# Performance work log

Measured on AMD Instinct MI355X. Metric: run time of the kernel, lower is better.

## Reference

```python
import jax, jax.numpy as jnp
import numpy as np
from jax import lax

B, T, O, E, I = 256, 16, 32, 32, 32
H, HL = 64, 64  # edge_dim, latent_edge_dim
TE, EI = T * E, E + I


def _mlp(x, layers):
    for w, b in layers[:-1]:
        x = jax.nn.relu(x @ w + b)
    w, b = layers[-1]
    return x @ w + b


def _get_edges(x, layers):
    # x: [B, O, D]; antisymmetric pairwise aggregation over upper-triangular pairs
    Bn, On, D = x.shape
    ii, jj = np.triu_indices(On, 1)  # static indices, P = O(O-1)/2
    pair_in = jnp.concatenate([x[:, ii, :], x[:, jj, :]], axis=-1)  # [B, P, 2D]
    e = _mlp(pair_in, layers)  # [B, P, H_out]
    agg = jnp.zeros((Bn, On, e.shape[-1]), x.dtype)
    agg = agg.at[:, ii, :].add(e).at[:, jj, :].add(-e)
    return agg


def setup_inputs() -> dict:
    key = jax.random.key(0)
    ks = iter(jax.random.split(key, 64))

    def lin(din, dout):
        w = jax.random.normal(next(ks), (din, dout), jnp.float32) * (1.0 / np.sqrt(din)).astype(np.float32)
        b = jnp.zeros((dout,), jnp.float32)
        return w, b

    inp = {"z_explicit_seq": jax.random.normal(next(ks), (B, T, O, E), jnp.float32)}
    groups = {
        "ee": [(2 * TE, 64), (64, 64), (64, H)],
        "ne": [(TE + H, 64), (64, 64), (64, 32), (32, I)],
        "le": [(2 * EI, 64), (64, 64), (64, HL)],
        "lt": [(EI + HL, 64), (64, 64), (64, 32), (32, 16), (16, EI)],
    }
    for name, dims in groups.items():
        for k, (din, dout) in enumerate(dims, start=1):
            w, b = lin(din, dout)
            inp[f"{name}{k}_w"] = w
            inp[f"{name}{k}_b"] = b
    inp["t_future"] = 8
    return inp


def reference(z_explicit_seq,
              ee1_w, ee1_b, ee2_w, ee2_b, ee3_w, ee3_b,
              ne1_w, ne1_b, ne2_w, ne2_b, ne3_w, ne3_b, ne4_w, ne4_b,
              le1_w, le1_b, le2_w, le2_b, le3_w, le3_b,
              lt1_w, lt1_b, lt2_w, lt2_b, lt3_w, lt3_b, lt4_w, lt4_b, lt5_w, lt5_b,
              t_future):
    ee = [(ee1_w, ee1_b), (ee2_w, ee2_b), (ee3_w, ee3_b)]
    ne = [(ne1_w, ne1_b), (ne2_w, ne2_b), (ne3_w, ne3_b), (ne4_w, ne4_b)]
    le = [(le1_w, le1_b), (le2_w, le2_b), (le3_w, le3_b)]
    lt = [(lt1_w, lt1_b), (lt2_w, lt2_b), (lt3_w, lt3_b), (lt4_w, lt4_b), (lt5_w, lt5_b)]

    z = z_explicit_seq  # [B, T, O, E]
    # define_source: first frame + temporal diffs, flatten time into features
    src = jnp.concatenate([z[:, :1], z[:, 1:] - z[:, :-1]], axis=1)  # [B,T,O,E]
    src = jnp.transpose(src, (0, 2, 1, 3)).reshape(B, O, TE)  # [B,O,TE]

    edge_agg = _get_edges(src, ee)  # [B,O,H]
    z_impl = _mlp(jnp.concatenate([src, edge_agg], axis=-1), ne)  # [B,O,I]
    z_cur = jnp.concatenate([z[:, -1], z_impl], axis=-1)  # [B,O,EI]

    def step(zc, _):
        agg = _get_edges(zc, le)  # [B,O,HL]
        delta = _mlp(jnp.concatenate([zc, agg], axis=-1), lt)  # [B,O,EI]
        zn = zc + delta
        return zn, zn[..., :E]

    _, preds = lax.scan(step, z_cur, None, length=t_future)  # [t,B,O,E]
    return jnp.transpose(preds, (1, 0, 2, 3))  # [B,t_future,O,E]
```

## Files before the change

### kernel.cpp

```cpp
#include <hip/hip_runtime.h>

#define NB 256
#define NO 32
#define NEE 32
#define NT 16
#define THREADS 512

typedef const float* __restrict__ fp;

struct Params {
  fp z;
  fp ee1w, ee1b, ee2w, ee2b, ee3w, ee3b;
  fp ne1w, ne1b, ne2w, ne2b, ne3w, ne3b, ne4w, ne4b;
  fp le1w, le1b, le2w, le2b, le3w, le3b;
  fp lt1w, lt1b, lt2w, lt2b, lt3w, lt3b, lt4w, lt4b, lt5w, lt5b;
  float* out;
  int tf;
};

__device__ __forceinline__ float frelu(float x) { return x > 0.f ? x : 0.f; }

__device__ __forceinline__ float rl(float v, int l) {
  return __uint_as_float(__builtin_amdgcn_readlane(__float_as_uint(v), l));
}

#define OFF_UT  0
#define OFF_VT  2112
#define OFF_AG  4224
#define OFF_BN  6272
#define OFF_NW  8320
#define LDSF    16000

__device__ __forceinline__ void stageN(float* dst, const float* __restrict__ src,
                                       int nf4, int tid) {
  for (int i4 = tid; i4 < nf4; i4 += THREADS)
    *(float4*)(dst + i4 * 4) = *(const float4*)(src + i4 * 4);
}

template<int KC>
__device__ __forceinline__ void dense4L(const float* x0, const float* x1,
                                        const float* x2, const float* x3,
                                        const float* __restrict__ w, int ldw,
                                        int col, float o[4]) {
#pragma unroll 4
  for (int kc = 0; kc < KC; ++kc) {
    float w0 = w[(4 * kc + 0) * ldw + col];
    float w1 = w[(4 * kc + 1) * ldw + col];
    float w2 = w[(4 * kc + 2) * ldw + col];
    float w3 = w[(4 * kc + 3) * ldw + col];
    float4 a = *(const float4*)(x0 + 4 * kc);
    float4 b = *(const float4*)(x1 + 4 * kc);
    float4 c = *(const float4*)(x2 + 4 * kc);
    float4 d = *(const float4*)(x3 + 4 * kc);
    o[0] = fmaf(a.x, w0, o[0]); o[0] = fmaf(a.y, w1, o[0]); o[0] = fmaf(a.z, w2, o[0]); o[0] = fmaf(a.w, w3, o[0]);
    o[1] = fmaf(b.x, w0, o[1]); o[1] = fmaf(b.y, w1, o[1]); o[1] = fmaf(b.z, w2, o[1]); o[1] = fmaf(b.w, w3, o[1]);
    o[2] = fmaf(c.x, w0, o[2]); o[2] = fmaf(c.y, w1, o[2]); o[2] = fmaf(c.z, w2, o[2]); o[2] = fmaf(c.w, w3, o[2]);
    o[3] = fmaf(d.x, w0, o[3]); o[3] = fmaf(d.y, w1, o[3]); o[3] = fmaf(d.z, w2, o[3]); o[3] = fmaf(d.w, w3, o[3]);
  }
}

__global__ __attribute__((amdgpu_waves_per_eu(2, 2)))
__launch_bounds__(THREADS) void rld_kernel(Params P) {
  __shared__ float lds[LDSF];
  const int b = blockIdx.x;
  const int tid = (int)threadIdx.x;
  const int lane = tid & 63;
  const int wave = tid >> 6;
  const int cc = lane & 31;
  const int c16 = lane & 15;

  float* UT = lds + OFF_UT;
  float* VT = lds + OFF_VT;
  float* AG = lds + OFF_AG;
  float* sBn = lds + OFF_BN + wave * 256;
  float* src = lds + OFF_BN;
  const float* wlt2 = lds + OFF_NW;
  const float* wlt3 = lds + OFF_NW + 4096;
  const float* wlt4 = lds + OFF_NW + 6144;
  const float* wlt5 = lds + OFF_NW + 6656;
  const int i0 = wave, i1 = wave + 8, i2 = wave + 16, i3 = wave + 24;
  const int h33 = lane * 33;
  const float* zb = P.z + (size_t)b * NT * NO * NEE;

  stageN(lds + OFF_NW,        P.lt2w, 1024, tid);
  stageN(lds + OFF_NW + 4096, P.lt3w,  512, tid);
  stageN(lds + OFF_NW + 6144, P.lt4w,  128, tid);
  stageN(lds + OFF_NW + 6656, P.lt5w,  256, tid);

  float au[4] = {0,0,0,0}, av[4] = {0,0,0,0}, s1r[4] = {0,0,0,0};
  for (int qq = 0; qq < 8; ++qq) {
    __syncthreads();
    for (int idx = tid; idx < 2048; idx += THREADS) {
      int i = idx >> 6, kk = idx & 63;
      int k = qq * 64 + kk, t = k >> 5, e = k & 31;
      float v = zb[(t * NO + i) * NEE + e];
      if (t > 0) v -= zb[((t - 1) * NO + i) * NEE + e];
      src[i * 64 + kk] = v;
    }
    __syncthreads();
    for (int c = 0; c < 2; ++c) {
      int r0 = qq * 64 + c * 32;
      const float* x0 = src + i0 * 64 + c * 32;
      const float* x1 = src + i1 * 64 + c * 32;
      const float* x2 = src + i2 * 64 + c * 32;
      const float* x3 = src + i3 * 64 + c * 32;
      dense4L<8>(x0, x1, x2, x3, P.ee1w + (size_t)r0 * 64,         64, lane, au);
      dense4L<8>(x0, x1, x2, x3, P.ee1w + (size_t)(512 + r0) * 64, 64, lane, av);
      dense4L<8>(x0, x1, x2, x3, P.ne1w + (size_t)r0 * 64,         64, lane, s1r);
    }
  }
  {
    float eb1 = P.ee1b[lane];
    UT[h33 + i0] = au[0] + eb1; UT[h33 + i1] = au[1] + eb1;
    UT[h33 + i2] = au[2] + eb1; UT[h33 + i3] = au[3] + eb1;
    VT[h33 + i0] = av[0]; VT[h33 + i1] = av[1];
    VT[h33 + i2] = av[2]; VT[h33 + i3] = av[3];
  }
  for (int z = tid; z < 2048; z += THREADS) AG[z] = 0.f;

  float w2c[64], w3c[64];
#pragma unroll
  for (int h = 0; h < 64; ++h) w2c[h] = P.ee2w[h * 64 + lane];
#pragma unroll
  for (int h = 0; h < 64; ++h) w3c[h] = P.ee3w[h * 64 + lane];
  float b2c = P.ee2b[lane], b3c = P.ee3b[lane];
  __syncthreads();

  const int tf = P.tf;
  float zci[4] = {0, 0, 0, 0};
  float* outb = P.out + (size_t)b * tf * NO * NEE;

  for (int s = 0; s <= tf; ++s) {
    {
      int pi = 0, rem = wave * 62;
      while (rem >= 31 - pi) { rem -= 31 - pi; ++pi; }
      int pj = pi + 1 + rem;
#pragma unroll 1
      for (int pp = 0; pp < 31; ++pp) {
        const int iA = pi, jA = pj;
        ++pj; if (pj == 32) { ++pi; pj = pi + 1; }
        const int iB = pi, jB = pj;
        ++pj; if (pj == 32) { ++pi; pj = pi + 1; }
        float xA = fmaxf(UT[h33 + iA] + VT[h33 + jA], 0.f);
        float xB = fmaxf(UT[h33 + iB] + VT[h33 + jB], 0.f);
        float a0 = b2c, a1 = 0.f, c0 = b2c, c1 = 0.f;
#pragma unroll
        for (int h = 0; h < 64; h += 2) {
          a0 = fmaf(rl(xA, h),     w2c[h],     a0);
          a1 = fmaf(rl(xA, h + 1), w2c[h + 1], a1);
          c0 = fmaf(rl(xB, h),     w2c[h],     c0);
          c1 = fmaf(rl(xB, h + 1), w2c[h + 1], c1);
        }
        float yA = fmaxf(a0 + a1, 0.f);
        float yB = fmaxf(c0 + c1, 0.f);
        float e0 = b3c, e1 = 0.f, f0 = b3c, f1 = 0.f;
#pragma unroll
        for (int h = 0; h < 64; h += 2) {
          e0 = fmaf(rl(yA, h),     w3c[h],     e0);
          e1 = fmaf(rl(yA, h + 1), w3c[h + 1], e1);
          f0 = fmaf(rl(yB, h),     w3c[h],     f0);
          f1 = fmaf(rl(yB, h + 1), w3c[h + 1], f1);
        }
        float eA = e0 + e1, eB = f0 + f1;
        atomicAdd(&AG[iA * 64 + lane],  eA);
        atomicAdd(&AG[jA * 64 + lane], -eA);
        atomicAdd(&AG[iB * 64 + lane],  eB);
        atomicAdd(&AG[jB * 64 + lane], -eB);
      }
    }
    __syncthreads();

    if (s == 0) {
      float nb1 = P.ne1b[lane], nb2 = P.ne2b[lane];
      float nb3 = P.ne3b[cc],   nb4 = P.ne4b[cc];
      float o1[4] = {s1r[0] + nb1, s1r[1] + nb1, s1r[2] + nb1, s1r[3] + nb1};
      dense4L<16>(AG + i0 * 64, AG + i1 * 64, AG + i2 * 64, AG + i3 * 64,
                  P.ne1w + (size_t)512 * 64, 64, lane, o1);
      sBn[lane] = frelu(o1[0]); sBn[64 + lane] = frelu(o1[1]);
      sBn[128 + lane] = frelu(o1[2]); sBn[192 + lane] = frelu(o1[3]);
      float o2[4] = {nb2, nb2, nb2, nb2};
      dense4L<16>(sBn, sBn + 64, sBn + 128, sBn + 192, P.ne2w, 64, lane, o2);
      sBn[lane] = frelu(o2[0]); sBn[64 + lane] = frelu(o2[1]);
      sBn[128 + lane] = frelu(o2[2]); sBn[192 + lane] = frelu(o2[3]);
      float o3[4] = {nb3, nb3, nb3, nb3};
      dense4L<16>(sBn, sBn + 64, sBn + 128, sBn + 192, P.ne3w, 32, cc, o3);
      sBn[cc] = frelu(o3[0]); sBn[64 + cc] = frelu(o3[1]);
      sBn[128 + cc] = frelu(o3[2]); sBn[192 + cc] = frelu(o3[3]);
      float o4[4] = {nb4, nb4, nb4, nb4};
      dense4L<8>(sBn, sBn + 64, sBn + 128, sBn + 192, P.ne4w, 32, cc, o4);
      zci[0] = (lane < 32) ? zb[(15 * NO + i0) * NEE + lane] : o4[0];
      zci[1] = (lane < 32) ? zb[(15 * NO + i1) * NEE + lane] : o4[1];
      zci[2] = (lane < 32) ? zb[(15 * NO + i2) * NEE + lane] : o4[2];
      zci[3] = (lane < 32) ? zb[(15 * NO + i3) * NEE + lane] : o4[3];
    } else {
      float lb1 = P.lt1b[lane], lb2 = P.lt2b[lane];
      float lb3 = P.lt3b[cc],   lb4 = P.lt4b[c16], lb5 = P.lt5b[lane];
      float o1[4] = {lb1, lb1, lb1, lb1};
      dense4L<16>(sBn, sBn + 64, sBn + 128, sBn + 192, P.lt1w, 64, lane, o1);
      dense4L<16>(AG + i0 * 64, AG + i1 * 64, AG + i2 * 64, AG + i3 * 64,
                  P.lt1w + (size_t)64 * 64, 64, lane, o1);
      sBn[lane] = frelu(o1[0]); sBn[64 + lane] = frelu(o1[1]);
      sBn[128 + lane] = frelu(o1[2]); sBn[192 + lane] = frelu(o1[3]);
      float o2[4] = {lb2, lb2, lb2, lb2};
      dense4L<16>(sBn, sBn + 64, sBn + 128, sBn + 192, wlt2, 64, lane, o2);
      sBn[lane] = frelu(o2[0]); sBn[64 + lane] = frelu(o2[1]);
      sBn[128 + lane] = frelu(o2[2]); sBn[192 + lane] = frelu(o2[3]);
      float o3[4] = {lb3, lb3, lb3, lb3};
      dense4L<16>(sBn, sBn + 64, sBn + 128, sBn + 192, wlt3, 32, cc, o3);
      sBn[cc] = frelu(o3[0]); sBn[64 + cc] = frelu(o3[1]);
      sBn[128 + cc] = frelu(o3[2]); sBn[192 + cc] = frelu(o3[3]);
      float o4[4] = {lb4, lb4, lb4, lb4};
      dense4L<8>(sBn, sBn + 64, sBn + 128, sBn + 192, wlt4, 16, c16, o4);
      sBn[c16] = frelu(o4[0]); sBn[64 + c16] = frelu(o4[1]);
      sBn[128 + c16] = frelu(o4[2]); sBn[192 + c16] = frelu(o4[3]);
      float o5[4] = {lb5, lb5, lb5, lb5};
      dense4L<4>(sBn, sBn + 64, sBn + 128, sBn + 192, wlt5, 64, lane, o5);
      zci[0] += o5[0]; zci[1] += o5[1]; zci[2] += o5[2]; zci[3] += o5[3];
      int t = s - 1;
      if (lane < 32) {
        outb[(t * NO + i0) * NEE + lane] = zci[0];
        outb[(t * NO + i1) * NEE + lane] = zci[1];
        outb[(t * NO + i2) * NEE + lane] = zci[2];
        outb[(t * NO + i3) * NEE + lane] = zci[3];
      }
    }
    __syncthreads();

    if (s < tf) {
      if (s == 0) {
#pragma unroll
        for (int h = 0; h < 64; ++h) w2c[h] = P.le2w[h * 64 + lane];
#pragma unroll
        for (int h = 0; h < 64; ++h) w3c[h] = P.le3w[h * 64 + lane];
        b2c = P.le2b[lane]; b3c = P.le3b[lane];
      }
      for (int z = tid; z < 2048; z += THREADS) AG[z] = 0.f;
      sBn[lane] = zci[0]; sBn[64 + lane] = zci[1];
      sBn[128 + lane] = zci[2]; sBn[192 + lane] = zci[3];
      float gb1 = P.le1b[lane];
      float ou[4] = {0,0,0,0}, ov[4] = {0,0,0,0};
      dense4L<16>(sBn, sBn + 64, sBn + 128, sBn + 192, P.le1w,        64, lane, ou);
      dense4L<16>(sBn, sBn + 64, sBn + 128, sBn + 192, P.le1w + 4096, 64, lane, ov);
      UT[h33 + i0] = ou[0] + gb1; UT[h33 + i1] = ou[1] + gb1;
      UT[h33 + i2] = ou[2] + gb1; UT[h33 + i3] = ou[3] + gb1;
      VT[h33 + i0] = ov[0]; VT[h33 + i1] = ov[1];
      VT[h33 + i2] = ov[2]; VT[h33 + i3] = ov[3];
    }
    __syncthreads();
  }
}

extern "C" void kernel_launch(void* const* d_in, const int* in_sizes, int n_in,
                              void* d_out, int out_size, void* d_ws, size_t ws_size,
                              hipStream_t stream) {
  (void)in_sizes; (void)n_in; (void)d_ws; (void)ws_size;
  Params P;
  int q = 0;
  P.z    = (fp)d_in[q++];
  P.ee1w = (fp)d_in[q++]; P.ee1b = (fp)d_in[q++];
  P.ee2w = (fp)d_in[q++]; P.ee2b = (fp)d_in[q++];
  P.ee3w = (fp)d_in[q++]; P.ee3b = (fp)d_in[q++];
  P.ne1w = (fp)d_in[q++]; P.ne1b = (fp)d_in[q++];
  P.ne2w = (fp)d_in[q++]; P.ne2b = (fp)d_in[q++];
  P.ne3w = (fp)d_in[q++]; P.ne3b = (fp)d_in[q++];
  P.ne4w = (fp)d_in[q++]; P.ne4b = (fp)d_in[q++];
  P.le1w = (fp)d_in[q++]; P.le1b = (fp)d_in[q++];
  P.le2w = (fp)d_in[q++]; P.le2b = (fp)d_in[q++];
  P.le3w = (fp)d_in[q++]; P.le3b = (fp)d_in[q++];
  P.lt1w = (fp)d_in[q++]; P.lt1b = (fp)d_in[q++];
  P.lt2w = (fp)d_in[q++]; P.lt2b = (fp)d_in[q++];
  P.lt3w = (fp)d_in[q++]; P.lt3b = (fp)d_in[q++];
  P.lt4w = (fp)d_in[q++]; P.lt4b = (fp)d_in[q++];
  P.lt5w = (fp)d_in[q++]; P.lt5b = (fp)d_in[q++];
  P.out = (float*)d_out;
  P.tf = out_size / (NB * NO * NEE);
  if (P.tf < 1) P.tf = 1;
  hipLaunchKernelGGL(rld_kernel, dim3(NB), dim3(THREADS), 0, stream, P);
}
```

Before: 1.165 ms.

## Split edge MLP into producer/consumer waves with double-buffered LDS hidden activations

```diff
diff --git a/kernel.cpp b/kernel.cpp
--- a/kernel.cpp
+++ b/kernel.cpp
@@ -1,4 +1,5 @@
 #include <hip/hip_runtime.h>
+#include <math.h>
 
 #define NB 256
 #define NO 32
@@ -24,18 +25,21 @@
   return __uint_as_float(__builtin_amdgcn_readlane(__float_as_uint(v), l));
 }
 
+__device__ __forceinline__ void unrank(int r, int& io, int& jo) {
+  float dd = (float)(3969 - 8 * r);
+  int i = (int)((63.0f - sqrtf(dd)) * 0.5f);
+  int off = i * (63 - i) / 2;
+  if (r < off) { --i; off = i * (63 - i) / 2; }
+  else { int off2 = (i + 1) * (62 - i) / 2; if (r >= off2) { ++i; off = off2; } }
+  io = i; jo = r - off + i + 1;
+}
+
 #define OFF_UT  0
 #define OFF_VT  2112
 #define OFF_AG  4224
 #define OFF_BN  6272
-#define OFF_NW  8320
-#define LDSF    16000
-
-__device__ __forceinline__ void stageN(float* dst, const float* __restrict__ src,
-                                       int nf4, int tid) {
-  for (int i4 = tid; i4 < nf4; i4 += THREADS)
-    *(float4*)(dst + i4 * 4) = *(const float4*)(src + i4 * 4);
-}
+#define OFF_Y   8320
+#define LDSF    16256
 
 template<int KC>
 __device__ __forceinline__ void dense4L(const float* x0, const float* x1,
@@ -59,8 +63,7 @@
   }
 }
 
-__global__ __attribute__((amdgpu_waves_per_eu(2, 2)))
-__launch_bounds__(THREADS) void rld_kernel(Params P) {
+__global__ __launch_bounds__(THREADS) void rld_kernel(Params P) {
   __shared__ float lds[LDSF];
   const int b = blockIdx.x;
   const int tid = (int)threadIdx.x;
@@ -68,24 +71,17 @@
   const int wave = tid >> 6;
   const int cc = lane & 31;
   const int c16 = lane & 15;
+  const int w4 = wave & 3;
+  const bool prod = wave < 4;
 
   float* UT = lds + OFF_UT;
   float* VT = lds + OFF_VT;
   float* AG = lds + OFF_AG;
   float* sBn = lds + OFF_BN + wave * 256;
   float* src = lds + OFF_BN;
-  const float* wlt2 = lds + OFF_NW;
-  const float* wlt3 = lds + OFF_NW + 4096;
-  const float* wlt4 = lds + OFF_NW + 6144;
-  const float* wlt5 = lds + OFF_NW + 6656;
   const int i0 = wave, i1 = wave + 8, i2 = wave + 16, i3 = wave + 24;
   const int h33 = lane * 33;
   const float* zb = P.z + (size_t)b * NT * NO * NEE;
-
-  stageN(lds + OFF_NW,        P.lt2w, 1024, tid);
-  stageN(lds + OFF_NW + 4096, P.lt3w,  512, tid);
-  stageN(lds + OFF_NW + 6144, P.lt4w,  128, tid);
-  stageN(lds + OFF_NW + 6656, P.lt5w,  256, tid);
 
   float au[4] = {0,0,0,0}, av[4] = {0,0,0,0}, s1r[4] = {0,0,0,0};
   for (int qq = 0; qq < 8; ++qq) {
@@ -118,57 +114,81 @@
   }
   for (int z = tid; z < 2048; z += THREADS) AG[z] = 0.f;
 
-  float w2c[64], w3c[64];
-#pragma unroll
-  for (int h = 0; h < 64; ++h) w2c[h] = P.ee2w[h * 64 + lane];
-#pragma unroll
-  for (int h = 0; h < 64; ++h) w3c[h] = P.ee3w[h * 64 + lane];
-  float b2c = P.ee2b[lane], b3c = P.ee3b[lane];
+  float wc[64], bc;
+  {
+    fp ws = prod ? P.ee2w : P.ee3w;
+#pragma unroll
+    for (int h = 0; h < 64; ++h) wc[h] = ws[h * 64 + lane];
+    bc = prod ? P.ee2b[lane] : P.ee3b[lane];
+  }
   __syncthreads();
 
   const int tf = P.tf;
   float zci[4] = {0, 0, 0, 0};
   float* outb = P.out + (size_t)b * tf * NO * NEE;
 
-  for (int s = 0; s <= tf; ++s) {
-    {
-      int pi = 0, rem = wave * 62;
-      while (rem >= 31 - pi) { rem -= 31 - pi; ++pi; }
-      int pj = pi + 1 + rem;
+  auto produce = [&](int cp) {
+    float* Yb = lds + OFF_Y + (cp & 1) * 3968;
 #pragma unroll 1
-      for (int pp = 0; pp < 31; ++pp) {
-        const int iA = pi, jA = pj;
-        ++pj; if (pj == 32) { ++pi; pj = pi + 1; }
-        const int iB = pi, jB = pj;
-        ++pj; if (pj == 32) { ++pi; pj = pi + 1; }
-        float xA = fmaxf(UT[h33 + iA] + VT[h33 + jA], 0.f);
-        float xB = fmaxf(UT[h33 + iB] + VT[h33 + jB], 0.f);
-        float a0 = b2c, a1 = 0.f, c0 = b2c, c1 = 0.f;
-#pragma unroll
-        for (int h = 0; h < 64; h += 2) {
-          a0 = fmaf(rl(xA, h),     w2c[h],     a0);
-          a1 = fmaf(rl(xA, h + 1), w2c[h + 1], a1);
-          c0 = fmaf(rl(xB, h),     w2c[h],     c0);
-          c1 = fmaf(rl(xB, h + 1), w2c[h + 1], c1);
-        }
-        float yA = fmaxf(a0 + a1, 0.f);
-        float yB = fmaxf(c0 + c1, 0.f);
-        float e0 = b3c, e1 = 0.f, f0 = b3c, f1 = 0.f;
-#pragma unroll
-        for (int h = 0; h < 64; h += 2) {
-          e0 = fmaf(rl(yA, h),     w3c[h],     e0);
-          e1 = fmaf(rl(yA, h + 1), w3c[h + 1], e1);
-          f0 = fmaf(rl(yB, h),     w3c[h],     f0);
-          f1 = fmaf(rl(yB, h + 1), w3c[h + 1], f1);
-        }
-        float eA = e0 + e1, eB = f0 + f1;
-        atomicAdd(&AG[iA * 64 + lane],  eA);
-        atomicAdd(&AG[jA * 64 + lane], -eA);
+    for (int t = 0; t < 8; ++t) {
+      int sA = w4 + 8 * t, sB = sA + 4;
+      bool vB = sB < 62;
+      int sB2 = vB ? sB : sA;
+      int iA, jA, iB, jB;
+      unrank(cp * 62 + sA, iA, jA);
+      unrank(cp * 62 + sB2, iB, jB);
+      float xA = fmaxf(UT[h33 + iA] + VT[h33 + jA], 0.f);
+      float xB = fmaxf(UT[h33 + iB] + VT[h33 + jB], 0.f);
+      float a0 = bc, a1 = 0.f, c0 = bc, c1 = 0.f;
+#pragma unroll
+      for (int h = 0; h < 64; h += 2) {
+        a0 = fmaf(rl(xA, h),     wc[h],     a0);
+        a1 = fmaf(rl(xA, h + 1), wc[h + 1], a1);
+        c0 = fmaf(rl(xB, h),     wc[h],     c0);
+        c1 = fmaf(rl(xB, h + 1), wc[h + 1], c1);
+      }
+      Yb[sA * 64 + lane] = fmaxf(a0 + a1, 0.f);
+      if (vB) Yb[sB * 64 + lane] = fmaxf(c0 + c1, 0.f);
+    }
+  };
+  auto consume = [&](int ch) {
+    const float* Yb = lds + OFF_Y + (ch & 1) * 3968;
+#pragma unroll 1
+    for (int t = 0; t < 8; ++t) {
+      int sA = w4 + 8 * t, sB = sA + 4;
+      bool vB = sB < 62;
+      int sB2 = vB ? sB : sA;
+      int iA, jA, iB, jB;
+      unrank(ch * 62 + sA, iA, jA);
+      unrank(ch * 62 + sB2, iB, jB);
+      float yA = Yb[sA * 64 + lane];
+      float yB = Yb[sB2 * 64 + lane];
+      float e0 = bc, e1 = 0.f, f0 = bc, f1 = 0.f;
+#pragma unroll
+      for (int h = 0; h < 64; h += 2) {
+        e0 = fmaf(rl(yA, h),     wc[h],     e0);
+        e1 = fmaf(rl(yA, h + 1), wc[h + 1], e1);
+        f0 = fmaf(rl(yB, h),     wc[h],     f0);
+        f1 = fmaf(rl(yB, h + 1), wc[h + 1], f1);
+      }
+      float eA = e0 + e1, eB = f0 + f1;
+      atomicAdd(&AG[iA * 64 + lane],  eA);
+      atomicAdd(&AG[jA * 64 + lane], -eA);
+      if (vB) {
         atomicAdd(&AG[iB * 64 + lane],  eB);
         atomicAdd(&AG[jB * 64 + lane], -eB);
       }
     }
-    __syncthreads();
+  };
+
+  for (int s = 0; s <= tf; ++s) {
+    if (prod) produce(0);
+    __syncthreads();
+    for (int ch = 0; ch < 8; ++ch) {
+      if (prod) { if (ch < 7) produce(ch + 1); }
+      else consume(ch);
+      __syncthreads();
+    }
 
     if (s == 0) {
       float nb1 = P.ne1b[lane], nb2 = P.ne2b[lane];
@@ -202,19 +222,19 @@
       sBn[lane] = frelu(o1[0]); sBn[64 + lane] = frelu(o1[1]);
       sBn[128 + lane] = frelu(o1[2]); sBn[192 + lane] = frelu(o1[3]);
       float o2[4] = {lb2, lb2, lb2, lb2};
-      dense4L<16>(sBn, sBn + 64, sBn + 128, sBn + 192, wlt2, 64, lane, o2);
+      dense4L<16>(sBn, sBn + 64, sBn + 128, sBn + 192, P.lt2w, 64, lane, o2);
       sBn[lane] = frelu(o2[0]); sBn[64 + lane] = frelu(o2[1]);
       sBn[128 + lane] = frelu(o2[2]); sBn[192 + lane] = frelu(o2[3]);
       float o3[4] = {lb3, lb3, lb3, lb3};
-      dense4L<16>(sBn, sBn + 64, sBn + 128, sBn + 192, wlt3, 32, cc, o3);
+      dense4L<16>(sBn, sBn + 64, sBn + 128, sBn + 192, P.lt3w, 32, cc, o3);
       sBn[cc] = frelu(o3[0]); sBn[64 + cc] = frelu(o3[1]);
       sBn[128 + cc] = frelu(o3[2]); sBn[192 + cc] = frelu(o3[3]);
       float o4[4] = {lb4, lb4, lb4, lb4};
-      dense4L<8>(sBn, sBn + 64, sBn + 128, sBn + 192, wlt4, 16, c16, o4);
+      dense4L<8>(sBn, sBn + 64, sBn + 128, sBn + 192, P.lt4w, 16, c16, o4);
       sBn[c16] = frelu(o4[0]); sBn[64 + c16] = frelu(o4[1]);
       sBn[128 + c16] = frelu(o4[2]); sBn[192 + c16] = frelu(o4[3]);
       float o5[4] = {lb5, lb5, lb5, lb5};
-      dense4L<4>(sBn, sBn + 64, sBn + 128, sBn + 192, wlt5, 64, lane, o5);
+      dense4L<4>(sBn, sBn + 64, sBn + 128, sBn + 192, P.lt5w, 64, lane, o5);
       zci[0] += o5[0]; zci[1] += o5[1]; zci[2] += o5[2]; zci[3] += o5[3];
       int t = s - 1;
       if (lane < 32) {
@@ -228,11 +248,10 @@
 
     if (s < tf) {
       if (s == 0) {
-#pragma unroll
-        for (int h = 0; h < 64; ++h) w2c[h] = P.le2w[h * 64 + lane];
-#pragma unroll
-        for (int h = 0; h < 64; ++h) w3c[h] = P.le3w[h * 64 + lane];
-        b2c = P.le2b[lane]; b3c = P.le3b[lane];
+        fp ws = prod ? P.le2w : P.le3w;
+#pragma unroll
+        for (int h = 0; h < 64; ++h) wc[h] = ws[h * 64 + lane];
+        bc = prod ? P.le2b[lane] : P.le3b[lane];
       }
       for (int z = tid; z < 2048; z += THREADS) AG[z] = 0.f;
       sBn[lane] = zci[0]; sBn[64 + lane] = zci[1];
```

Result: slower. 1.551 ms (+33.2%).

## Double block size to 1024 threads and split rows across sixteen waves

Applied to the files above, without the earlier changes.

```diff
diff --git a/kernel.cpp b/kernel.cpp
--- a/kernel.cpp
+++ b/kernel.cpp
@@ -4,7 +4,7 @@
 #define NO 32
 #define NEE 32
 #define NT 16
-#define THREADS 512
+#define THREADS 1024
 
 typedef const float* __restrict__ fp;
 
@@ -38,10 +38,9 @@
 }
 
 template<int KC>
-__device__ __forceinline__ void dense4L(const float* x0, const float* x1,
-                                        const float* x2, const float* x3,
+__device__ __forceinline__ void dense2L(const float* x0, const float* x1,
                                         const float* __restrict__ w, int ldw,
-                                        int col, float o[4]) {
+                                        int col, float o[2]) {
 #pragma unroll 4
   for (int kc = 0; kc < KC; ++kc) {
     float w0 = w[(4 * kc + 0) * ldw + col];
@@ -50,17 +49,12 @@
     float w3 = w[(4 * kc + 3) * ldw + col];
     float4 a = *(const float4*)(x0 + 4 * kc);
     float4 b = *(const float4*)(x1 + 4 * kc);
-    float4 c = *(const float4*)(x2 + 4 * kc);
-    float4 d = *(const float4*)(x3 + 4 * kc);
     o[0] = fmaf(a.x, w0, o[0]); o[0] = fmaf(a.y, w1, o[0]); o[0] = fmaf(a.z, w2, o[0]); o[0] = fmaf(a.w, w3, o[0]);
     o[1] = fmaf(b.x, w0, o[1]); o[1] = fmaf(b.y, w1, o[1]); o[1] = fmaf(b.z, w2, o[1]); o[1] = fmaf(b.w, w3, o[1]);
-    o[2] = fmaf(c.x, w0, o[2]); o[2] = fmaf(c.y, w1, o[2]); o[2] = fmaf(c.z, w2, o[2]); o[2] = fmaf(c.w, w3, o[2]);
-    o[3] = fmaf(d.x, w0, o[3]); o[3] = fmaf(d.y, w1, o[3]); o[3] = fmaf(d.z, w2, o[3]); o[3] = fmaf(d.w, w3, o[3]);
-  }
-}
-
-__global__ __attribute__((amdgpu_waves_per_eu(2, 2)))
-__launch_bounds__(THREADS) void rld_kernel(Params P) {
+  }
+}
+
+__global__ __launch_bounds__(THREADS) void rld_kernel(Params P) {
   __shared__ float lds[LDSF];
   const int b = blockIdx.x;
   const int tid = (int)threadIdx.x;
@@ -72,13 +66,13 @@
   float* UT = lds + OFF_UT;
   float* VT = lds + OFF_VT;
   float* AG = lds + OFF_AG;
-  float* sBn = lds + OFF_BN + wave * 256;
+  float* sBn = lds + OFF_BN + wave * 128;
   float* src = lds + OFF_BN;
   const float* wlt2 = lds + OFF_NW;
   const float* wlt3 = lds + OFF_NW + 4096;
   const float* wlt4 = lds + OFF_NW + 6144;
   const float* wlt5 = lds + OFF_NW + 6656;
-  const int i0 = wave, i1 = wave + 8, i2 = wave + 16, i3 = wave + 24;
+  const int i0 = wave, i1 = wave + 16;
   const int h33 = lane * 33;
   const float* zb = P.z + (size_t)b * NT * NO * NEE;
 
@@ -87,7 +81,7 @@
   stageN(lds + OFF_NW + 6144, P.lt4w,  128, tid);
   stageN(lds + OFF_NW + 6656, P.lt5w,  256, tid);
 
-  float au[4] = {0,0,0,0}, av[4] = {0,0,0,0}, s1r[4] = {0,0,0,0};
+  float au[2] = {0,0}, av[2] = {0,0}, s1r[2] = {0,0};
   for (int qq = 0; qq < 8; ++qq) {
     __syncthreads();
     for (int idx = tid; idx < 2048; idx += THREADS) {
@@ -102,19 +96,15 @@
       int r0 = qq * 64 + c * 32;
       const float* x0 = src + i0 * 64 + c * 32;
       const float* x1 = src + i1 * 64 + c * 32;
-      const float* x2 = src + i2 * 64 + c * 32;
-      const float* x3 = src + i3 * 64 + c * 32;
-      dense4L<8>(x0, x1, x2, x3, P.ee1w + (size_t)r0 * 64,         64, lane, au);
-      dense4L<8>(x0, x1, x2, x3, P.ee1w + (size_t)(512 + r0) * 64, 64, lane, av);
-      dense4L<8>(x0, x1, x2, x3, P.ne1w + (size_t)r0 * 64,         64, lane, s1r);
+      dense2L<8>(x0, x1, P.ee1w + (size_t)r0 * 64,         64, lane, au);
+      dense2L<8>(x0, x1, P.ee1w + (size_t)(512 + r0) * 64, 64, lane, av);
+      dense2L<8>(x0, x1, P.ne1w + (size_t)r0 * 64,         64, lane, s1r);
     }
   }
   {
     float eb1 = P.ee1b[lane];
     UT[h33 + i0] = au[0] + eb1; UT[h33 + i1] = au[1] + eb1;
-    UT[h33 + i2] = au[2] + eb1; UT[h33 + i3] = au[3] + eb1;
-    VT[h33 + i0] = av[0]; VT[h33 + i1] = av[1];
-    VT[h33 + i2] = av[2]; VT[h33 + i3] = av[3];
+    VT[h33 + i0] = av[0];      VT[h33 + i1] = av[1];
   }
   for (int z = tid; z < 2048; z += THREADS) AG[z] = 0.f;
 
@@ -127,16 +117,16 @@
   __syncthreads();
 
   const int tf = P.tf;
-  float zci[4] = {0, 0, 0, 0};
+  float zci[2] = {0, 0};
   float* outb = P.out + (size_t)b * tf * NO * NEE;
 
   for (int s = 0; s <= tf; ++s) {
     {
-      int pi = 0, rem = wave * 62;
+      int pi = 0, rem = wave * 31;
       while (rem >= 31 - pi) { rem -= 31 - pi; ++pi; }
       int pj = pi + 1 + rem;
 #pragma unroll 1
-      for (int pp = 0; pp < 31; ++pp) {
+      for (int pp = 0; pp < 15; ++pp) {
         const int iA = pi, jA = pj;
         ++pj; if (pj == 32) { ++pi; pj = pi + 1; }
         const int iB = pi, jB = pj;
@@ -167,61 +157,68 @@
         atomicAdd(&AG[iB * 64 + lane],  eB);
         atomicAdd(&AG[jB * 64 + lane], -eB);
       }
+      {
+        const int iA = pi, jA = pj;
+        float xA = fmaxf(UT[h33 + iA] + VT[h33 + jA], 0.f);
+        float a0 = b2c, a1 = 0.f;
+#pragma unroll
+        for (int h = 0; h < 64; h += 2) {
+          a0 = fmaf(rl(xA, h),     w2c[h],     a0);
+          a1 = fmaf(rl(xA, h + 1), w2c[h + 1], a1);
+        }
+        float yA = fmaxf(a0 + a1, 0.f);
+        float e0 = b3c, e1 = 0.f;
+#pragma unroll
+        for (int h = 0; h < 64; h += 2) {
+          e0 = fmaf(rl(yA, h),     w3c[h],     e0);
+          e1 = fmaf(rl(yA, h + 1), w3c[h + 1], e1);
+        }
+        float eA = e0 + e1;
+        atomicAdd(&AG[iA * 64 + lane],  eA);
+        atomicAdd(&AG[jA * 64 + lane], -eA);
+      }
     }
     __syncthreads();
 
     if (s == 0) {
       float nb1 = P.ne1b[lane], nb2 = P.ne2b[lane];
       float nb3 = P.ne3b[cc],   nb4 = P.ne4b[cc];
-      float o1[4] = {s1r[0] + nb1, s1r[1] + nb1, s1r[2] + nb1, s1r[3] + nb1};
-      dense4L<16>(AG + i0 * 64, AG + i1 * 64, AG + i2 * 64, AG + i3 * 64,
-                  P.ne1w + (size_t)512 * 64, 64, lane, o1);
+      float o1[2] = {s1r[0] + nb1, s1r[1] + nb1};
+      dense2L<16>(AG + i0 * 64, AG + i1 * 64, P.ne1w + (size_t)512 * 64, 64, lane, o1);
       sBn[lane] = frelu(o1[0]); sBn[64 + lane] = frelu(o1[1]);
-      sBn[128 + lane] = frelu(o1[2]); sBn[192 + lane] = frelu(o1[3]);
-      float o2[4] = {nb2, nb2, nb2, nb2};
-      dense4L<16>(sBn, sBn + 64, sBn + 128, sBn + 192, P.ne2w, 64, lane, o2);
+      float o2[2] = {nb2, nb2};
+      dense2L<16>(sBn, sBn + 64, P.ne2w, 64, lane, o2);
       sBn[lane] = frelu(o2[0]); sBn[64 + lane] = frelu(o2[1]);
-      sBn[128 + lane] = frelu(o2[2]); sBn[192 + lane] = frelu(o2[3]);
-      float o3[4] = {nb3, nb3, nb3, nb3};
-      dense4L<16>(sBn, sBn + 64, sBn + 128, sBn + 192, P.ne3w, 32, cc, o3);
+      float o3[2] = {nb3, nb3};
+      dense2L<16>(sBn, sBn + 64, P.ne3w, 32, cc, o3);
       sBn[cc] = frelu(o3[0]); sBn[64 + cc] = frelu(o3[1]);
-      sBn[128 + cc] = frelu(o3[2]); sBn[192 + cc] = frelu(o3[3]);
-      float o4[4] = {nb4, nb4, nb4, nb4};
-      dense4L<8>(sBn, sBn + 64, sBn + 128, sBn + 192, P.ne4w, 32, cc, o4);
+      float o4[2] = {nb4, nb4};
+      dense2L<8>(sBn, sBn + 64, P.ne4w, 32, cc, o4);
       zci[0] = (lane < 32) ? zb[(15 * NO + i0) * NEE + lane] : o4[0];
       zci[1] = (lane < 32) ? zb[(15 * NO + i1) * NEE + lane] : o4[1];
-      zci[2] = (lane < 32) ? zb[(15 * NO + i2) * NEE + lane] : o4[2];
-      zci[3] = (lane < 32) ? zb[(15 * NO + i3) * NEE + lane] : o4[3];
     } else {
       float lb1 = P.lt1b[lane], lb2 = P.lt2b[lane];
       float lb3 = P.lt3b[cc],   lb4 = P.lt4b[c16], lb5 = P.lt5b[lane];
-      float o1[4] = {lb1, lb1, lb1, lb1};
-      dense4L<16>(sBn, sBn + 64, sBn + 128, sBn + 192, P.lt1w, 64, lane, o1);
-      dense4L<16>(AG + i0 * 64, AG + i1 * 64, AG + i2 * 64, AG + i3 * 64,
-                  P.lt1w + (size_t)64 * 64, 64, lane, o1);
+      float o1[2] = {lb1, lb1};
+      dense2L<16>(sBn, sBn + 64, P.lt1w, 64, lane, o1);
+      dense2L<16>(AG + i0 * 64, AG + i1 * 64, P.lt1w + (size_t)64 * 64, 64, lane, o1);
       sBn[lane] = frelu(o1[0]); sBn[64 + lane] = frelu(o1[1]);
-      sBn[128 + lane] = frelu(o1[2]); sBn[192 + lane] = frelu(o1[3]);
-      float o2[4] = {lb2, lb2, lb2, lb2};
-      dense4L<16>(sBn, sBn + 64, sBn + 128, sBn + 192, wlt2, 64, lane, o2);
+      float o2[2] = {lb2, lb2};
+      dense2L<16>(sBn, sBn + 64, wlt2, 64, lane, o2);
       sBn[lane] = frelu(o2[0]); sBn[64 + lane] = frelu(o2[1]);
-      sBn[128 + lane] = frelu(o2[2]); sBn[192 + lane] = frelu(o2[3]);
-      float o3[4] = {lb3, lb3, lb3, lb3};
-      dense4L<16>(sBn, sBn + 64, sBn + 128, sBn + 192, wlt3, 32, cc, o3);
+      float o3[2] = {lb3, lb3};
+      dense2L<16>(sBn, sBn + 64, wlt3, 32, cc, o3);
       sBn[cc] = frelu(o3[0]); sBn[64 + cc] = frelu(o3[1]);
-      sBn[128 + cc] = frelu(o3[2]); sBn[192 + cc] = frelu(o3[3]);
-      float o4[4] = {lb4, lb4, lb4, lb4};
-      dense4L<8>(sBn, sBn + 64, sBn + 128, sBn + 192, wlt4, 16, c16, o4);
+      float o4[2] = {lb4, lb4};
+      dense2L<8>(sBn, sBn + 64, wlt4, 16, c16, o4);
       sBn[c16] = frelu(o4[0]); sBn[64 + c16] = frelu(o4[1]);
-      sBn[128 + c16] = frelu(o4[2]); sBn[192 + c16] = frelu(o4[3]);
-      float o5[4] = {lb5, lb5, lb5, lb5};
-      dense4L<4>(sBn, sBn + 64, sBn + 128, sBn + 192, wlt5, 64, lane, o5);
-      zci[0] += o5[0]; zci[1] += o5[1]; zci[2] += o5[2]; zci[3] += o5[3];
+      float o5[2] = {lb5, lb5};
+      dense2L<4>(sBn, sBn + 64, wlt5, 64, lane, o5);
+      zci[0] += o5[0]; zci[1] += o5[1];
       int t = s - 1;
       if (lane < 32) {
         outb[(t * NO + i0) * NEE + lane] = zci[0];
         outb[(t * NO + i1) * NEE + lane] = zci[1];
-        outb[(t * NO + i2) * NEE + lane] = zci[2];
-        outb[(t * NO + i3) * NEE + lane] = zci[3];
       }
     }
     __syncthreads();
@@ -236,15 +233,12 @@
       }
       for (int z = tid; z < 2048; z += THREADS) AG[z] = 0.f;
       sBn[lane] = zci[0]; sBn[64 + lane] = zci[1];
-      sBn[128 + lane] = zci[2]; sBn[192 + lane] = zci[3];
       float gb1 = P.le1b[lane];
-      float ou[4] = {0,0,0,0}, ov[4] = {0,0,0,0};
-      dense4L<16>(sBn, sBn + 64, sBn + 128, sBn + 192, P.le1w,        64, lane, ou);
-      dense4L<16>(sBn, sBn + 64, sBn + 128, sBn + 192, P.le1w + 4096, 64, lane, ov);
+      float ou[2] = {0,0}, ov[2] = {0,0};
+      dense2L<16>(sBn, sBn + 64, P.le1w,        64, lane, ou);
+      dense2L<16>(sBn, sBn + 64, P.le1w + 4096, 64, lane, ov);
       UT[h33 + i0] = ou[0] + gb1; UT[h33 + i1] = ou[1] + gb1;
-      UT[h33 + i2] = ou[2] + gb1; UT[h33 + i3] = ou[3] + gb1;
-      VT[h33 + i0] = ov[0]; VT[h33 + i1] = ov[1];
-      VT[h33 + i2] = ov[2]; VT[h33 + i3] = ov[3];
+      VT[h33 + i0] = ov[0];       VT[h33 + i1] = ov[1];
     }
     __syncthreads();
   }
```

After: 3.695 ms. 217% more time.

## Move third edge-MLP weights from registers to transposed LDS and drop waves_per_eu

Applied to the files above, without the earlier changes.

```diff
diff --git a/kernel.cpp b/kernel.cpp
--- a/kernel.cpp
+++ b/kernel.cpp
@@ -28,13 +28,16 @@
 #define OFF_VT  2112
 #define OFF_AG  4224
 #define OFF_BN  6272
-#define OFF_NW  8320
-#define LDSF    16000
-
-__device__ __forceinline__ void stageN(float* dst, const float* __restrict__ src,
-                                       int nf4, int tid) {
-  for (int i4 = tid; i4 < nf4; i4 += THREADS)
-    *(float4*)(dst + i4 * 4) = *(const float4*)(src + i4 * 4);
+#define OFF_W3T 8320
+#define LDSF    12544
+
+__device__ __forceinline__ void stageW3T(float* lds, fp w3, int tid) {
+#pragma unroll
+  for (int r = 0; r < 8; ++r) {
+    int idx = tid + r * THREADS;
+    int h = idx >> 6, c = idx & 63;
+    lds[OFF_W3T + c * 66 + h] = w3[h * 64 + c];
+  }
 }
 
 template<int KC>
@@ -59,8 +62,7 @@
   }
 }
 
-__global__ __attribute__((amdgpu_waves_per_eu(2, 2)))
-__launch_bounds__(THREADS) void rld_kernel(Params P) {
+__global__ __launch_bounds__(THREADS) void rld_kernel(Params P) {
   __shared__ float lds[LDSF];
   const int b = blockIdx.x;
   const int tid = (int)threadIdx.x;
@@ -74,18 +76,11 @@
   float* AG = lds + OFF_AG;
   float* sBn = lds + OFF_BN + wave * 256;
   float* src = lds + OFF_BN;
-  const float* wlt2 = lds + OFF_NW;
-  const float* wlt3 = lds + OFF_NW + 4096;
-  const float* wlt4 = lds + OFF_NW + 6144;
-  const float* wlt5 = lds + OFF_NW + 6656;
   const int i0 = wave, i1 = wave + 8, i2 = wave + 16, i3 = wave + 24;
   const int h33 = lane * 33;
   const float* zb = P.z + (size_t)b * NT * NO * NEE;
 
-  stageN(lds + OFF_NW,        P.lt2w, 1024, tid);
-  stageN(lds + OFF_NW + 4096, P.lt3w,  512, tid);
-  stageN(lds + OFF_NW + 6144, P.lt4w,  128, tid);
-  stageN(lds + OFF_NW + 6656, P.lt5w,  256, tid);
+  stageW3T(lds, P.ee3w, tid);
 
   float au[4] = {0,0,0,0}, av[4] = {0,0,0,0}, s1r[4] = {0,0,0,0};
   for (int qq = 0; qq < 8; ++qq) {
@@ -118,11 +113,9 @@
   }
   for (int z = tid; z < 2048; z += THREADS) AG[z] = 0.f;
 
-  float w2c[64], w3c[64];
+  float w2c[64];
 #pragma unroll
   for (int h = 0; h < 64; ++h) w2c[h] = P.ee2w[h * 64 + lane];
-#pragma unroll
-  for (int h = 0; h < 64; ++h) w3c[h] = P.ee3w[h * 64 + lane];
   float b2c = P.ee2b[lane], b3c = P.ee3b[lane];
   __syncthreads();
 
@@ -135,6 +128,7 @@
       int pi = 0, rem = wave * 62;
       while (rem >= 31 - pi) { rem -= 31 - pi; ++pi; }
       int pj = pi + 1 + rem;
+      const float* w3row = lds + OFF_W3T + lane * 66;
 #pragma unroll 1
       for (int pp = 0; pp < 31; ++pp) {
         const int iA = pi, jA = pj;
@@ -156,10 +150,11 @@
         float e0 = b3c, e1 = 0.f, f0 = b3c, f1 = 0.f;
 #pragma unroll
         for (int h = 0; h < 64; h += 2) {
-          e0 = fmaf(rl(yA, h),     w3c[h],     e0);
-          e1 = fmaf(rl(yA, h + 1), w3c[h + 1], e1);
-          f0 = fmaf(rl(yB, h),     w3c[h],     f0);
-          f1 = fmaf(rl(yB, h + 1), w3c[h + 1], f1);
+          float2 wp = *(const float2*)(w3row + h);
+          e0 = fmaf(rl(yA, h),     wp.x, e0);
+          e1 = fmaf(rl(yA, h + 1), wp.y, e1);
+          f0 = fmaf(rl(yB, h),     wp.x, f0);
+          f1 = fmaf(rl(yB, h + 1), wp.y, f1);
         }
         float eA = e0 + e1, eB = f0 + f1;
         atomicAdd(&AG[iA * 64 + lane],  eA);
@@ -202,19 +197,19 @@
       sBn[lane] = frelu(o1[0]); sBn[64 + lane] = frelu(o1[1]);
       sBn[128 + lane] = frelu(o1[2]); sBn[192 + lane] = frelu(o1[3]);
       float o2[4] = {lb2, lb2, lb2, lb2};
-      dense4L<16>(sBn, sBn + 64, sBn + 128, sBn + 192, wlt2, 64, lane, o2);
+      dense4L<16>(sBn, sBn + 64, sBn + 128, sBn + 192, P.lt2w, 64, lane, o2);
       sBn[lane] = frelu(o2[0]); sBn[64 + lane] = frelu(o2[1]);
       sBn[128 + lane] = frelu(o2[2]); sBn[192 + lane] = frelu(o2[3]);
       float o3[4] = {lb3, lb3, lb3, lb3};
-      dense4L<16>(sBn, sBn + 64, sBn + 128, sBn + 192, wlt3, 32, cc, o3);
+      dense4L<16>(sBn, sBn + 64, sBn + 128, sBn + 192, P.lt3w, 32, cc, o3);
       sBn[cc] = frelu(o3[0]); sBn[64 + cc] = frelu(o3[1]);
       sBn[128 + cc] = frelu(o3[2]); sBn[192 + cc] = frelu(o3[3]);
       float o4[4] = {lb4, lb4, lb4, lb4};
-      dense4L<8>(sBn, sBn + 64, sBn + 128, sBn + 192, wlt4, 16, c16, o4);
+      dense4L<8>(sBn, sBn + 64, sBn + 128, sBn + 192, P.lt4w, 16, c16, o4);
       sBn[c16] = frelu(o4[0]); sBn[64 + c16] = frelu(o4[1]);
       sBn[128 + c16] = frelu(o4[2]); sBn[192 + c16] = frelu(o4[3]);
       float o5[4] = {lb5, lb5, lb5, lb5};
-      dense4L<4>(sBn, sBn + 64, sBn + 128, sBn + 192, wlt5, 64, lane, o5);
+      dense4L<4>(sBn, sBn + 64, sBn + 128, sBn + 192, P.lt5w, 64, lane, o5);
       zci[0] += o5[0]; zci[1] += o5[1]; zci[2] += o5[2]; zci[3] += o5[3];
       int t = s - 1;
       if (lane < 32) {
@@ -230,9 +225,8 @@
       if (s == 0) {
 #pragma unroll
         for (int h = 0; h < 64; ++h) w2c[h] = P.le2w[h * 64 + lane];
-#pragma unroll
-        for (int h = 0; h < 64; ++h) w3c[h] = P.le3w[h * 64 + lane];
         b2c = P.le2b[lane]; b3c = P.le3b[lane];
+        stageW3T(lds, P.le3w, tid);
       }
       for (int z = tid; z < 2048; z += THREADS) AG[z] = 0.f;
       sBn[lane] = zci[0]; sBn[64 + lane] = zci[1];
```

Result: slower. 1.598 ms (+37.2%).
